# Optimization experiments

Measured on AMD Instinct MI355X. Metric: run time of the kernel, lower is better.

## Reference

```python
import jax, jax.numpy as jnp
import numpy as np

B, N, D, W = 4, 4096, 256, 7
K = 2 * W + 1  # 15 taps: positions [i-2w, ..., i]
H = 4 * D
EPS = 1e-5


def layer_norm(x, g, b):
    mu = jnp.mean(x, axis=-1, keepdims=True)
    var = jnp.mean(jnp.square(x - mu), axis=-1, keepdims=True)
    return (x - mu) * jax.lax.rsqrt(var + EPS) * g + b


def setup_inputs() -> dict:
    key = jax.random.key(0)
    ks = jax.random.split(key, 8)
    s = 0.02
    return {
        "x": jax.random.normal(ks[0], (B, N, D), dtype=jnp.float32),
        # w_mix[k] is the DxD block of the (K*D -> D) Linear acting on offset k-2w
        "w_mix": (jax.random.normal(ks[1], (K, D, D), dtype=jnp.float32) * s),
        "b_mix": jnp.zeros((D,), dtype=jnp.float32),
        "g1": jnp.ones((D,), jnp.float32) + 0.1 * jax.random.normal(ks[2], (D,), jnp.float32),
        "b1": 0.1 * jax.random.normal(ks[3], (D,), jnp.float32),
        "w_ff1": jax.random.normal(ks[4], (D, H), dtype=jnp.float32) * s,
        "b_ff1": jnp.zeros((H,), dtype=jnp.float32),
        "w_ff2": jax.random.normal(ks[5], (H, D), dtype=jnp.float32) * s,
        "b_ff2": jnp.zeros((D,), dtype=jnp.float32),
        "g2": jnp.ones((D,), jnp.float32) + 0.1 * jax.random.normal(ks[6], (D,), jnp.float32),
        "b2": 0.1 * jax.random.normal(ks[7], (D,), jnp.float32),
    }


def reference(x, w_mix, b_mix, g1, b1, w_ff1, b_ff1, w_ff2, b_ff2, g2, b2):
    # Causal windowed concat + Linear == causal 1D conv with kernel K=2w+1.
    # torch feats chunk k holds x[i - 2w + k]; conv tap k with left pad 2w
    # sees exactly x[i - 2w + k], so kernel = mix weight reshaped (K, D, D).
    mix = jax.lax.conv_general_dilated(
        x, w_mix, window_strides=(1,), padding=[(2 * W, 0)],
        dimension_numbers=("NWC", "WIO", "NWC"),
    ) + b_mix  # [B, N, D]
    # Dropout is identity in eval mode (reference baseline).
    h = layer_norm(x + mix, g1, b1)
    ff = jnp.dot(jax.nn.gelu(jnp.dot(h, w_ff1) + b_ff1, approximate=False), w_ff2) + b_ff2
    return layer_norm(h + ff, g2, b2)
```

## Files before the change

kernel.cpp:

```cpp
#include <hip/hip_runtime.h>
#include <cstdint>

#define DD     256
#define HH     1024
#define NNSEQ  4096
#define MT     32
#define XR     46
#define XPITCH 264
#define SLOTP  260
#define EPSLN  1e-5f

typedef unsigned short u16;
typedef __attribute__((ext_vector_type(8))) short short8;
typedef __attribute__((ext_vector_type(4))) float f32x4;

#define MFMA(a, b, c) __builtin_amdgcn_mfma_f32_16x16x32_bf16(a, b, c, 0, 0, 0)

__device__ __forceinline__ u16 f2bf(float f) {
  unsigned u = __float_as_uint(f);
  u += 0x7FFF + ((u >> 16) & 1);
  return (u16)(u >> 16);
}
__device__ __forceinline__ float bf2f(u16 s) { return __uint_as_float(((unsigned)s) << 16); }

__device__ __forceinline__ float fast_gelu(float v) {
  const float e = __expf(v * __builtin_fmaf(v * v, -0.0713548163f, -1.5957691216f));
  return v * __builtin_amdgcn_rcpf(1.f + e);
}

__global__ __launch_bounds__(256) void k_prep(
    const float* __restrict__ wmix, const float* __restrict__ wff1,
    const float* __restrict__ wff2, u16* __restrict__ wpk,
    u16* __restrict__ w1pk, u16* __restrict__ w2pk)
{
  const int g = blockIdx.x * 256 + threadIdx.x;
  const int u = g >> 10;
  const int t = g & 1023;
  const int fi = t >> 6, l = t & 63, q = l >> 4, cl = l & 15;
  const int n = fi * 16 + cl;
  const int r0 = q * 8;

  const float* src;
  int rowstride;
  u16* dst;
  if (u < 120) {
    src = wmix + (size_t)(u * 32 + r0) * 256 + n;
    rowstride = 256;
    dst = wpk + (size_t)u * 8192;
  } else if (u < 152) {
    const int v = u - 120, c2 = v >> 3, s = v & 7;
    src = wff1 + (size_t)(s * 32 + r0) * 1024 + c2 * 256 + n;
    rowstride = 1024;
    dst = w1pk + (size_t)v * 8192;
  } else {
    const int v = u - 152, c2 = v >> 3, s = v & 7;
    src = wff2 + (size_t)(c2 * 256 + s * 32 + r0) * 256 + n;
    rowstride = 256;
    dst = w2pk + (size_t)v * 8192;
  }

  float w[8];
#pragma unroll
  for (int j = 0; j < 8; ++j) w[j] = src[(size_t)j * rowstride];

  uint4 pk;
  unsigned* p = (unsigned*)&pk;
#pragma unroll
  for (int jj = 0; jj < 4; ++jj)
    p[jj] = (unsigned)f2bf(w[jj * 2]) | ((unsigned)f2bf(w[jj * 2 + 1]) << 16);
  *(uint4*)&dst[(size_t)fi * 512 + (size_t)l * 8] = pk;
}

__global__ __launch_bounds__(512, 4) void k_fused(
    const float* __restrict__ x, const u16* __restrict__ wpk,
    const float* __restrict__ bmix, const float* __restrict__ g1,
    const float* __restrict__ b1, const u16* __restrict__ w1pk,
    const float* __restrict__ bf1, const u16* __restrict__ w2pk,
    const float* __restrict__ bf2, const float* __restrict__ g2,
    const float* __restrict__ b2, float* __restrict__ out)
{
  __shared__ __align__(16) u16 bufA[XR * XPITCH];
  __shared__ __align__(16) u16 asbuf[2 * MT * XPITCH];
  __shared__ float redS[8][MT], redS2[8][MT];
  __shared__ float muL[MT], invL[MT];

#define bufB ((float*)asbuf)

  const int tid = threadIdx.x;
  const int wv = tid >> 6, l = tid & 63, q = l >> 4, cl = l & 15;
  const int mg = wv >> 2, ng = wv & 3;
  const long tok0 = (long)blockIdx.x * MT;
  const int n0 = (int)(tok0 & (NNSEQ - 1));

  f32x4 acc[2][4];
#pragma unroll
  for (int nt = 0; nt < 4; ++nt) {
    const float bm = (mg == 0) ? bmix[ng * 64 + nt * 16 + cl] : 0.f;
#pragma unroll
    for (int mt = 0; mt < 2; ++mt) acc[mt][nt] = (f32x4){bm, bm, bm, bm};
  }
  const u16* bbase = wpk + (size_t)(mg * 60) * 8192 + (size_t)(ng * 4) * 512 + (size_t)l * 8;

  {
    const int cslot = l * 4;
    for (int r = wv; r < XR; r += 8) {
      const int nloc = n0 - 14 + r;
      float4 v = make_float4(0.f, 0.f, 0.f, 0.f);
      if (nloc >= 0) v = *(const float4*)&x[(tok0 - 14 + r) * DD + cslot];
      uint2 pk;
      pk.x = (unsigned)f2bf(v.x) | ((unsigned)f2bf(v.y) << 16);
      pk.y = (unsigned)f2bf(v.z) | ((unsigned)f2bf(v.w) << 16);
      *(uint2*)&bufA[r * XPITCH + cslot] = pk;
    }
  }

#define LOAD_A(dst, s_)                                                         \
  {                                                                             \
    const int ks = mg * 60 + (s_);                                              \
    const int xrow = ks >> 3, c0 = (ks & 7) * 32;                               \
    _Pragma("unroll")                                                           \
    for (int mt = 0; mt < 2; ++mt)                                              \
      dst[mt] = *(const short8*)&bufA[(xrow + mt * 16 + cl) * XPITCH + c0 + q * 8]; \
  }
#define LOAD_B(dst, s_)                                                         \
  {                                                                             \
    const u16* bp = bbase + (size_t)(s_) * 8192;                                \
    _Pragma("unroll")                                                           \
    for (int nt = 0; nt < 4; ++nt)                                              \
      dst[nt] = *(const short8*)(bp + nt * 512);                                \
  }

  {
    short8 af[3][2], bfr[3][4];
    LOAD_B(bfr[0], 0)
    LOAD_B(bfr[1], 1)
    LOAD_B(bfr[2], 2)
    __syncthreads();
    LOAD_A(af[0], 0)
    LOAD_A(af[1], 1)
    LOAD_A(af[2], 2)

    for (int sb = 0; sb < 57; sb += 3) {
#pragma unroll
      for (int u = 0; u < 3; ++u) {
#pragma unroll
        for (int mt = 0; mt < 2; ++mt)
#pragma unroll
          for (int nt = 0; nt < 4; ++nt)
            acc[mt][nt] = MFMA(af[u][mt], bfr[u][nt], acc[mt][nt]);
        LOAD_A(af[u], sb + u + 3)
        LOAD_B(bfr[u], sb + u + 3)
      }
    }
#pragma unroll
    for (int u = 0; u < 3; ++u) {
#pragma unroll
      for (int mt = 0; mt < 2; ++mt)
#pragma unroll
        for (int nt = 0; nt < 4; ++nt)
          acc[mt][nt] = MFMA(af[u][mt], bfr[u][nt], acc[mt][nt]);
    }
  }
#undef LOAD_A
#undef LOAD_B

  if (mg == 1) {
#pragma unroll
    for (int mt = 0; mt < 2; ++mt)
#pragma unroll
      for (int nt = 0; nt < 4; ++nt)
#pragma unroll
        for (int reg = 0; reg < 4; ++reg)
          bufB[(mt * 16 + q * 4 + reg) * SLOTP + ng * 64 + nt * 16 + cl] = acc[mt][nt][reg];
  }
  __syncthreads();

  if (mg == 0) {
    float ps[2][4], ps2[2][4];
#pragma unroll
    for (int mt = 0; mt < 2; ++mt)
#pragma unroll
      for (int reg = 0; reg < 4; ++reg) {
        const int row = mt * 16 + q * 4 + reg;
        float s = 0.f, s2 = 0.f;
#pragma unroll
        for (int nt = 0; nt < 4; ++nt) {
          const int col = ng * 64 + nt * 16 + cl;
          const float y = acc[mt][nt][reg] + bufB[row * SLOTP + col]
                        + x[(tok0 + row) * DD + col];
          acc[mt][nt][reg] = y;
          s += y; s2 += y * y;
        }
#pragma unroll
        for (int off = 1; off < 16; off <<= 1) { s += __shfl_xor(s, off, 64); s2 += __shfl_xor(s2, off, 64); }
        ps[mt][reg] = s; ps2[mt][reg] = s2;
      }
    if (cl == 0) {
#pragma unroll
      for (int mt = 0; mt < 2; ++mt)
#pragma unroll
        for (int reg = 0; reg < 4; ++reg) {
          const int row = mt * 16 + q * 4 + reg;
          redS[ng][row] = ps[mt][reg]; redS2[ng][row] = ps2[mt][reg];
        }
    }
  }
  __syncthreads();
  if (tid < MT) {
    const float s  = redS[0][tid] + redS[1][tid] + redS[2][tid] + redS[3][tid];
    const float s2 = redS2[0][tid] + redS2[1][tid] + redS2[2][tid] + redS2[3][tid];
    const float mu = s * (1.f / DD);
    const float var = s2 * (1.f / DD) - mu * mu;
    muL[tid] = mu; invL[tid] = rsqrtf(var + EPSLN);
  }
  __syncthreads();

  if (mg == 0) {
#pragma unroll
    for (int nt = 0; nt < 4; ++nt) {
      const int col = ng * 64 + nt * 16 + cl;
      const float gv = g1[col], bv = b1[col];
#pragma unroll
      for (int mt = 0; mt < 2; ++mt)
#pragma unroll
        for (int reg = 0; reg < 4; ++reg) {
          const int row = mt * 16 + q * 4 + reg;
          const float hv = (acc[mt][nt][reg] - muL[row]) * invL[row] * gv + bv;
          bufA[row * XPITCH + col] = f2bf(hv);
        }
    }
  }
  __syncthreads();

  f32x4 acc2[2][2];
#pragma unroll
  for (int nt = 0; nt < 2; ++nt) {
    const float bv = bf2[wv * 32 + nt * 16 + cl];
#pragma unroll
    for (int mt = 0; mt < 2; ++mt) acc2[mt][nt] = (f32x4){bv, bv, bv, bv};
  }

#define FF_LDA(src, dst, s_)                                                    \
  {                                                                             \
    _Pragma("unroll")                                                           \
    for (int mt = 0; mt < 2; ++mt)                                              \
      dst[mt] = *(const short8*)&src[(mt * 16 + cl) * XPITCH + (s_) * 32 + q * 8]; \
  }
#define FF_LDB(wsrc, dst, s_)                                                   \
  {                                                                             \
    const u16* bp = wsrc + (size_t)(c * 8 + (s_)) * 8192 + (size_t)(wv * 2) * 512 + (size_t)l * 8; \
    _Pragma("unroll")                                                           \
    for (int nt = 0; nt < 2; ++nt)                                              \
      dst[nt] = *(const short8*)(bp + nt * 512);                                \
  }

  for (int c = 0; c < 4; ++c) {
    u16* asb = asbuf + (c & 1) * (MT * XPITCH);
    f32x4 acc1[2][2];
#pragma unroll
    for (int nt = 0; nt < 2; ++nt) {
      const float bv = bf1[c * 256 + wv * 32 + nt * 16 + cl];
#pragma unroll
      for (int mt = 0; mt < 2; ++mt) acc1[mt][nt] = (f32x4){bv, bv, bv, bv};
    }
    {
      short8 a2[2][2], b2r[2][2];
      FF_LDA(bufA, a2[0], 0) FF_LDB(w1pk, b2r[0], 0)
      FF_LDA(bufA, a2[1], 1) FF_LDB(w1pk, b2r[1], 1)
#pragma unroll
      for (int s = 0; s < 6; ++s) {
        const int cur = s & 1;
#pragma unroll
        for (int mt = 0; mt < 2; ++mt)
#pragma unroll
          for (int nt = 0; nt < 2; ++nt)
            acc1[mt][nt] = MFMA(a2[cur][mt], b2r[cur][nt], acc1[mt][nt]);
        FF_LDA(bufA, a2[cur], s + 2) FF_LDB(w1pk, b2r[cur], s + 2)
      }
#pragma unroll
      for (int s = 6; s < 8; ++s) {
        const int cur = s & 1;
#pragma unroll
        for (int mt = 0; mt < 2; ++mt)
#pragma unroll
          for (int nt = 0; nt < 2; ++nt)
            acc1[mt][nt] = MFMA(a2[cur][mt], b2r[cur][nt], acc1[mt][nt]);
      }
    }
#pragma unroll
    for (int mt = 0; mt < 2; ++mt)
#pragma unroll
      for (int nt = 0; nt < 2; ++nt)
#pragma unroll
        for (int reg = 0; reg < 4; ++reg) {
          const float g = fast_gelu(acc1[mt][nt][reg]);
          asb[(mt * 16 + q * 4 + reg) * XPITCH + wv * 32 + nt * 16 + cl] = f2bf(g);
        }
    __syncthreads();
    {
      short8 a2[2][2], b2r[2][2];
      FF_LDA(asb, a2[0], 0) FF_LDB(w2pk, b2r[0], 0)
      FF_LDA(asb, a2[1], 1) FF_LDB(w2pk, b2r[1], 1)
#pragma unroll
      for (int s = 0; s < 6; ++s) {
        const int cur = s & 1;
#pragma unroll
        for (int mt = 0; mt < 2; ++mt)
#pragma unroll
          for (int nt = 0; nt < 2; ++nt)
            acc2[mt][nt] = MFMA(a2[cur][mt], b2r[cur][nt], acc2[mt][nt]);
        FF_LDA(asb, a2[cur], s + 2) FF_LDB(w2pk, b2r[cur], s + 2)
      }
#pragma unroll
      for (int s = 6; s < 8; ++s) {
        const int cur = s & 1;
#pragma unroll
        for (int mt = 0; mt < 2; ++mt)
#pragma unroll
          for (int nt = 0; nt < 2; ++nt)
            acc2[mt][nt] = MFMA(a2[cur][mt], b2r[cur][nt], acc2[mt][nt]);
      }
    }
  }
#undef FF_LDA
#undef FF_LDB

  {
    float ps[2][4], ps2[2][4];
#pragma unroll
    for (int mt = 0; mt < 2; ++mt)
#pragma unroll
      for (int reg = 0; reg < 4; ++reg) {
        const int row = mt * 16 + q * 4 + reg;
        float s = 0.f, s2 = 0.f;
#pragma unroll
        for (int nt = 0; nt < 2; ++nt) {
          const int col = wv * 32 + nt * 16 + cl;
          const float y = acc2[mt][nt][reg] + bf2f(bufA[row * XPITCH + col]);
          acc2[mt][nt][reg] = y;
          s += y; s2 += y * y;
        }
#pragma unroll
        for (int off = 1; off < 16; off <<= 1) { s += __shfl_xor(s, off, 64); s2 += __shfl_xor(s2, off, 64); }
        ps[mt][reg] = s; ps2[mt][reg] = s2;
      }
    if (cl == 0) {
#pragma unroll
      for (int mt = 0; mt < 2; ++mt)
#pragma unroll
        for (int reg = 0; reg < 4; ++reg) {
          const int row = mt * 16 + q * 4 + reg;
          redS[wv][row] = ps[mt][reg]; redS2[wv][row] = ps2[mt][reg];
        }
    }
  }
  __syncthreads();
  if (tid < MT) {
    float s = 0.f, s2 = 0.f;
#pragma unroll
    for (int k = 0; k < 8; ++k) { s += redS[k][tid]; s2 += redS2[k][tid]; }
    const float mu = s * (1.f / DD);
    const float var = s2 * (1.f / DD) - mu * mu;
    muL[tid] = mu; invL[tid] = rsqrtf(var + EPSLN);
  }
  __syncthreads();

#pragma unroll
  for (int nt = 0; nt < 2; ++nt) {
    const int col = wv * 32 + nt * 16 + cl;
    const float gv = g2[col], bv = b2[col];
#pragma unroll
    for (int mt = 0; mt < 2; ++mt)
#pragma unroll
      for (int reg = 0; reg < 4; ++reg) {
        const int row = mt * 16 + q * 4 + reg;
        out[(tok0 + row) * DD + col] = (acc2[mt][nt][reg] - muL[row]) * invL[row] * gv + bv;
      }
  }
#undef bufB
}

extern "C" void kernel_launch(void* const* d_in, const int* in_sizes, int n_in,
                              void* d_out, int out_size, void* d_ws, size_t ws_size,
                              hipStream_t stream) {
  const float* x    = (const float*)d_in[0];
  const float* wmix = (const float*)d_in[1];
  const float* bmix = (const float*)d_in[2];
  const float* g1   = (const float*)d_in[3];
  const float* b1   = (const float*)d_in[4];
  const float* wff1 = (const float*)d_in[5];
  const float* bff1 = (const float*)d_in[6];
  const float* wff2 = (const float*)d_in[7];
  const float* bff2 = (const float*)d_in[8];
  const float* g2   = (const float*)d_in[9];
  const float* b2   = (const float*)d_in[10];
  float* out = (float*)d_out;

  u16* wpk  = (u16*)d_ws;
  u16* w1pk = wpk + 983040;
  u16* w2pk = w1pk + 262144;

  k_prep<<<736, 256, 0, stream>>>(wmix, wff1, wff2, wpk, w1pk, w2pk);

  k_fused<<<512, 512, 0, stream>>>(x, wpk, bmix, g1, b1,
                                   w1pk, bff1, w2pk, bff2, g2, b2, out);
}
```

Measured before the change: 153.5 us.

## Switch fused block to 32x32x16 MFMA with repacked weights and prefetch

Replaces the 16x16x32 bf16 MFMA tiling with 32x32x16 MFMA across the conv-mix, FF1 and FF2 GEMMs, and repacks the prep kernel's weight layout to match the 32-wide fragments. Each wave now issues fewer, larger MFMAs with fewer A/B fragment loads per flop. It also prefetches the next FF1/FF2 weight fragments across phase boundaries, hoists the residual x loads before the sync, and wraps the MFMAs in s_setprio. The row mapping changes, and the row reductions now need 32-lane shuffles instead of 16-lane ones.

```diff
diff --git a/kernel.cpp b/kernel.cpp
--- a/kernel.cpp
+++ b/kernel.cpp
@@ -12,9 +12,9 @@
 
 typedef unsigned short u16;
 typedef __attribute__((ext_vector_type(8))) short short8;
-typedef __attribute__((ext_vector_type(4))) float f32x4;
-
-#define MFMA(a, b, c) __builtin_amdgcn_mfma_f32_16x16x32_bf16(a, b, c, 0, 0, 0)
+typedef __attribute__((ext_vector_type(16))) float f32x16;
+
+#define MFMA32(a, b, c) __builtin_amdgcn_mfma_f32_32x32x16_bf16(a, b, c, 0, 0, 0)
 
 __device__ __forceinline__ u16 f2bf(float f) {
   unsigned u = __float_as_uint(f);
@@ -36,9 +36,10 @@
   const int g = blockIdx.x * 256 + threadIdx.x;
   const int u = g >> 10;
   const int t = g & 1023;
-  const int fi = t >> 6, l = t & 63, q = l >> 4, cl = l & 15;
-  const int n = fi * 16 + cl;
-  const int r0 = q * 8;
+  const int fp = t >> 6, l = t & 63;
+  const int gg = fp >> 1, h = fp & 1;
+  const int n = gg * 32 + (l & 31);
+  const int r0 = h * 16 + (l >> 5) * 8;
 
   const float* src;
   int rowstride;
@@ -68,7 +69,7 @@
 #pragma unroll
   for (int jj = 0; jj < 4; ++jj)
     p[jj] = (unsigned)f2bf(w[jj * 2]) | ((unsigned)f2bf(w[jj * 2 + 1]) << 16);
-  *(uint4*)&dst[(size_t)fi * 512 + (size_t)l * 8] = pk;
+  *(uint4*)&dst[(size_t)fp * 512 + (size_t)l * 8] = pk;
 }
 
 __global__ __launch_bounds__(512, 4) void k_fused(
@@ -87,19 +88,22 @@
 #define bufB ((float*)asbuf)
 
   const int tid = threadIdx.x;
-  const int wv = tid >> 6, l = tid & 63, q = l >> 4, cl = l & 15;
+  const int wv = tid >> 6, l = tid & 63;
+  const int l31 = l & 31, lh = l >> 5;
   const int mg = wv >> 2, ng = wv & 3;
   const long tok0 = (long)blockIdx.x * MT;
   const int n0 = (int)(tok0 & (NNSEQ - 1));
 
-  f32x4 acc[2][4];
-#pragma unroll
-  for (int nt = 0; nt < 4; ++nt) {
-    const float bm = (mg == 0) ? bmix[ng * 64 + nt * 16 + cl] : 0.f;
-#pragma unroll
-    for (int mt = 0; mt < 2; ++mt) acc[mt][nt] = (f32x4){bm, bm, bm, bm};
-  }
-  const u16* bbase = wpk + (size_t)(mg * 60) * 8192 + (size_t)(ng * 4) * 512 + (size_t)l * 8;
+#define ROWOF(r) (((r) & 3) + 8 * ((r) >> 2) + 4 * lh)
+
+  f32x16 acc[2];
+#pragma unroll
+  for (int nt = 0; nt < 2; ++nt) {
+    const float bm = (mg == 0) ? bmix[ng * 64 + nt * 32 + l31] : 0.f;
+#pragma unroll
+    for (int r = 0; r < 16; ++r) acc[nt][r] = bm;
+  }
+  const u16* bpkb = wpk + (size_t)(ng * 2048) + (size_t)l * 8;
 
   {
     const int cslot = l * 4;
@@ -114,95 +118,96 @@
     }
   }
 
-#define LOAD_A(dst, s_)                                                         \
+#define C_LOAD_A(dst, kg_)                                                      \
   {                                                                             \
-    const int ks = mg * 60 + (s_);                                              \
-    const int xrow = ks >> 3, c0 = (ks & 7) * 32;                               \
-    _Pragma("unroll")                                                           \
-    for (int mt = 0; mt < 2; ++mt)                                              \
-      dst[mt] = *(const short8*)&bufA[(xrow + mt * 16 + cl) * XPITCH + c0 + q * 8]; \
-  }
-#define LOAD_B(dst, s_)                                                         \
+    const int tap = (kg_) >> 4, c0 = ((kg_) & 15) * 16;                         \
+    dst = *(const short8*)&bufA[(tap + l31) * XPITCH + c0 + lh * 8];            \
+  }
+#define C_LOAD_B(dst, kg_)                                                      \
   {                                                                             \
-    const u16* bp = bbase + (size_t)(s_) * 8192;                                \
-    _Pragma("unroll")                                                           \
-    for (int nt = 0; nt < 4; ++nt)                                              \
-      dst[nt] = *(const short8*)(bp + nt * 512);                                \
-  }
-
-  {
-    short8 af[3][2], bfr[3][4];
-    LOAD_B(bfr[0], 0)
-    LOAD_B(bfr[1], 1)
-    LOAD_B(bfr[2], 2)
+    const u16* bp = bpkb + (size_t)((kg_) >> 1) * 8192 + (size_t)((kg_) & 1) * 512; \
+    dst[0] = *(const short8*)bp;                                                \
+    dst[1] = *(const short8*)(bp + 1024);                                       \
+  }
+
+  {
+    const int kg0 = mg * 120;
+    short8 af[4], bfr[4][2];
+    C_LOAD_B(bfr[0], kg0 + 0)
+    C_LOAD_B(bfr[1], kg0 + 1)
+    C_LOAD_B(bfr[2], kg0 + 2)
+    C_LOAD_B(bfr[3], kg0 + 3)
     __syncthreads();
-    LOAD_A(af[0], 0)
-    LOAD_A(af[1], 1)
-    LOAD_A(af[2], 2)
-
-    for (int sb = 0; sb < 57; sb += 3) {
-#pragma unroll
-      for (int u = 0; u < 3; ++u) {
-#pragma unroll
-        for (int mt = 0; mt < 2; ++mt)
-#pragma unroll
-          for (int nt = 0; nt < 4; ++nt)
-            acc[mt][nt] = MFMA(af[u][mt], bfr[u][nt], acc[mt][nt]);
-        LOAD_A(af[u], sb + u + 3)
-        LOAD_B(bfr[u], sb + u + 3)
-      }
-    }
-#pragma unroll
-    for (int u = 0; u < 3; ++u) {
-#pragma unroll
-      for (int mt = 0; mt < 2; ++mt)
-#pragma unroll
-        for (int nt = 0; nt < 4; ++nt)
-          acc[mt][nt] = MFMA(af[u][mt], bfr[u][nt], acc[mt][nt]);
-    }
-  }
-#undef LOAD_A
-#undef LOAD_B
+    C_LOAD_A(af[0], kg0 + 0)
+    C_LOAD_A(af[1], kg0 + 1)
+    C_LOAD_A(af[2], kg0 + 2)
+    C_LOAD_A(af[3], kg0 + 3)
+
+    for (int sb = 0; sb < 116; sb += 4) {
+#pragma unroll
+      for (int u = 0; u < 4; ++u) {
+        __builtin_amdgcn_s_setprio(1);
+        acc[0] = MFMA32(af[u], bfr[u][0], acc[0]);
+        acc[1] = MFMA32(af[u], bfr[u][1], acc[1]);
+        __builtin_amdgcn_s_setprio(0);
+        C_LOAD_A(af[u], kg0 + sb + u + 4)
+        C_LOAD_B(bfr[u], kg0 + sb + u + 4)
+      }
+    }
+#pragma unroll
+    for (int u = 0; u < 4; ++u) {
+      __builtin_amdgcn_s_setprio(1);
+      acc[0] = MFMA32(af[u], bfr[u][0], acc[0]);
+      acc[1] = MFMA32(af[u], bfr[u][1], acc[1]);
+      __builtin_amdgcn_s_setprio(0);
+    }
+  }
+#undef C_LOAD_A
+#undef C_LOAD_B
+
+  float xres[2][16];
+  if (mg == 0) {
+#pragma unroll
+    for (int r = 0; r < 16; ++r) {
+      const int row = ROWOF(r);
+      const float* xp = &x[(tok0 + row) * DD + ng * 64 + l31];
+      xres[0][r] = xp[0];
+      xres[1][r] = xp[32];
+    }
+  }
 
   if (mg == 1) {
 #pragma unroll
-    for (int mt = 0; mt < 2; ++mt)
-#pragma unroll
-      for (int nt = 0; nt < 4; ++nt)
-#pragma unroll
-        for (int reg = 0; reg < 4; ++reg)
-          bufB[(mt * 16 + q * 4 + reg) * SLOTP + ng * 64 + nt * 16 + cl] = acc[mt][nt][reg];
+    for (int nt = 0; nt < 2; ++nt)
+#pragma unroll
+      for (int r = 0; r < 16; ++r)
+        bufB[ROWOF(r) * SLOTP + ng * 64 + nt * 32 + l31] = acc[nt][r];
   }
   __syncthreads();
 
   if (mg == 0) {
-    float ps[2][4], ps2[2][4];
-#pragma unroll
-    for (int mt = 0; mt < 2; ++mt)
-#pragma unroll
-      for (int reg = 0; reg < 4; ++reg) {
-        const int row = mt * 16 + q * 4 + reg;
-        float s = 0.f, s2 = 0.f;
-#pragma unroll
-        for (int nt = 0; nt < 4; ++nt) {
-          const int col = ng * 64 + nt * 16 + cl;
-          const float y = acc[mt][nt][reg] + bufB[row * SLOTP + col]
-                        + x[(tok0 + row) * DD + col];
-          acc[mt][nt][reg] = y;
-          s += y; s2 += y * y;
-        }
-#pragma unroll
-        for (int off = 1; off < 16; off <<= 1) { s += __shfl_xor(s, off, 64); s2 += __shfl_xor(s2, off, 64); }
-        ps[mt][reg] = s; ps2[mt][reg] = s2;
-      }
-    if (cl == 0) {
-#pragma unroll
-      for (int mt = 0; mt < 2; ++mt)
-#pragma unroll
-        for (int reg = 0; reg < 4; ++reg) {
-          const int row = mt * 16 + q * 4 + reg;
-          redS[ng][row] = ps[mt][reg]; redS2[ng][row] = ps2[mt][reg];
-        }
+    float ps[16], ps2[16];
+#pragma unroll
+    for (int r = 0; r < 16; ++r) {
+      const int row = ROWOF(r);
+      float s = 0.f, s2 = 0.f;
+#pragma unroll
+      for (int nt = 0; nt < 2; ++nt) {
+        const int col = ng * 64 + nt * 32 + l31;
+        const float y = acc[nt][r] + bufB[row * SLOTP + col] + xres[nt][r];
+        acc[nt][r] = y;
+        s += y; s2 += y * y;
+      }
+#pragma unroll
+      for (int off = 1; off < 32; off <<= 1) { s += __shfl_xor(s, off, 64); s2 += __shfl_xor(s2, off, 64); }
+      ps[r] = s; ps2[r] = s2;
+    }
+    if (l31 == 0) {
+#pragma unroll
+      for (int r = 0; r < 16; ++r) {
+        const int row = ROWOF(r);
+        redS[ng][row] = ps[r]; redS2[ng][row] = ps2[r];
+      }
     }
   }
   __syncthreads();
@@ -215,143 +220,124 @@
   }
   __syncthreads();
 
+#define F_LDA(src, dst, s_)                                                     \
+    dst = *(const short8*)&src[l31 * XPITCH + (s_) * 16 + lh * 8];
+#define F_LDB(wsrc, dst, c_, s_)                                                \
+    dst = *(const short8*)(wsrc + (size_t)((c_) * 8 + ((s_) >> 1)) * 8192       \
+                          + (size_t)(wv * 2 + ((s_) & 1)) * 512 + (size_t)l * 8);
+
+  short8 pb1[3];
+  F_LDB(w1pk, pb1[0], 0, 0)
+  F_LDB(w1pk, pb1[1], 0, 1)
+  F_LDB(w1pk, pb1[2], 0, 2)
+
   if (mg == 0) {
 #pragma unroll
-    for (int nt = 0; nt < 4; ++nt) {
-      const int col = ng * 64 + nt * 16 + cl;
+    for (int nt = 0; nt < 2; ++nt) {
+      const int col = ng * 64 + nt * 32 + l31;
       const float gv = g1[col], bv = b1[col];
 #pragma unroll
-      for (int mt = 0; mt < 2; ++mt)
-#pragma unroll
-        for (int reg = 0; reg < 4; ++reg) {
-          const int row = mt * 16 + q * 4 + reg;
-          const float hv = (acc[mt][nt][reg] - muL[row]) * invL[row] * gv + bv;
-          bufA[row * XPITCH + col] = f2bf(hv);
-        }
-    }
-  }
-  __syncthreads();
-
-  f32x4 acc2[2][2];
-#pragma unroll
-  for (int nt = 0; nt < 2; ++nt) {
-    const float bv = bf2[wv * 32 + nt * 16 + cl];
-#pragma unroll
-    for (int mt = 0; mt < 2; ++mt) acc2[mt][nt] = (f32x4){bv, bv, bv, bv};
-  }
-
-#define FF_LDA(src, dst, s_)                                                    \
-  {                                                                             \
-    _Pragma("unroll")                                                           \
-    for (int mt = 0; mt < 2; ++mt)                                              \
-      dst[mt] = *(const short8*)&src[(mt * 16 + cl) * XPITCH + (s_) * 32 + q * 8]; \
-  }
-#define FF_LDB(wsrc, dst, s_)                                                   \
-  {                                                                             \
-    const u16* bp = wsrc + (size_t)(c * 8 + (s_)) * 8192 + (size_t)(wv * 2) * 512 + (size_t)l * 8; \
-    _Pragma("unroll")                                                           \
-    for (int nt = 0; nt < 2; ++nt)                                              \
-      dst[nt] = *(const short8*)(bp + nt * 512);                                \
+      for (int r = 0; r < 16; ++r) {
+        const int row = ROWOF(r);
+        bufA[row * XPITCH + col] = f2bf((acc[nt][r] - muL[row]) * invL[row] * gv + bv);
+      }
+    }
+  }
+  __syncthreads();
+
+  f32x16 acc2;
+  {
+    const float bv = bf2[wv * 32 + l31];
+#pragma unroll
+    for (int r = 0; r < 16; ++r) acc2[r] = bv;
   }
 
   for (int c = 0; c < 4; ++c) {
     u16* asb = asbuf + (c & 1) * (MT * XPITCH);
-    f32x4 acc1[2][2];
-#pragma unroll
-    for (int nt = 0; nt < 2; ++nt) {
-      const float bv = bf1[c * 256 + wv * 32 + nt * 16 + cl];
-#pragma unroll
-      for (int mt = 0; mt < 2; ++mt) acc1[mt][nt] = (f32x4){bv, bv, bv, bv};
-    }
+    f32x16 acc1;
     {
-      short8 a2[2][2], b2r[2][2];
-      FF_LDA(bufA, a2[0], 0) FF_LDB(w1pk, b2r[0], 0)
-      FF_LDA(bufA, a2[1], 1) FF_LDB(w1pk, b2r[1], 1)
-#pragma unroll
-      for (int s = 0; s < 6; ++s) {
-        const int cur = s & 1;
-#pragma unroll
-        for (int mt = 0; mt < 2; ++mt)
-#pragma unroll
-          for (int nt = 0; nt < 2; ++nt)
-            acc1[mt][nt] = MFMA(a2[cur][mt], b2r[cur][nt], acc1[mt][nt]);
-        FF_LDA(bufA, a2[cur], s + 2) FF_LDB(w1pk, b2r[cur], s + 2)
-      }
-#pragma unroll
-      for (int s = 6; s < 8; ++s) {
-        const int cur = s & 1;
-#pragma unroll
-        for (int mt = 0; mt < 2; ++mt)
-#pragma unroll
-          for (int nt = 0; nt < 2; ++nt)
-            acc1[mt][nt] = MFMA(a2[cur][mt], b2r[cur][nt], acc1[mt][nt]);
-      }
-    }
-#pragma unroll
-    for (int mt = 0; mt < 2; ++mt)
-#pragma unroll
-      for (int nt = 0; nt < 2; ++nt)
-#pragma unroll
-        for (int reg = 0; reg < 4; ++reg) {
-          const float g = fast_gelu(acc1[mt][nt][reg]);
-          asb[(mt * 16 + q * 4 + reg) * XPITCH + wv * 32 + nt * 16 + cl] = f2bf(g);
-        }
+      const float bv = bf1[c * 256 + wv * 32 + l31];
+#pragma unroll
+      for (int r = 0; r < 16; ++r) acc1[r] = bv;
+    }
+    {
+      short8 a3[3], b3[3];
+      F_LDA(bufA, a3[0], 0) b3[0] = pb1[0];
+      F_LDA(bufA, a3[1], 1) b3[1] = pb1[1];
+      F_LDA(bufA, a3[2], 2) b3[2] = pb1[2];
+#pragma unroll
+      for (int s = 0; s < 13; ++s) {
+        const int cur = s % 3;
+        __builtin_amdgcn_s_setprio(1);
+        acc1 = MFMA32(a3[cur], b3[cur], acc1);
+        __builtin_amdgcn_s_setprio(0);
+        F_LDA(bufA, a3[cur], s + 3)
+        F_LDB(w1pk, b3[cur], c, s + 3)
+      }
+      __builtin_amdgcn_s_setprio(1);
+#pragma unroll
+      for (int s = 13; s < 16; ++s)
+        acc1 = MFMA32(a3[s % 3], b3[s % 3], acc1);
+      __builtin_amdgcn_s_setprio(0);
+    }
+    short8 pb2[3];
+    F_LDB(w2pk, pb2[0], c, 0)
+    F_LDB(w2pk, pb2[1], c, 1)
+    F_LDB(w2pk, pb2[2], c, 2)
+#pragma unroll
+    for (int r = 0; r < 16; ++r) {
+      const float g = fast_gelu(acc1[r]);
+      asb[ROWOF(r) * XPITCH + wv * 32 + l31] = f2bf(g);
+    }
+    if (c < 3) {
+      F_LDB(w1pk, pb1[0], c + 1, 0)
+      F_LDB(w1pk, pb1[1], c + 1, 1)
+      F_LDB(w1pk, pb1[2], c + 1, 2)
+    }
     __syncthreads();
     {
-      short8 a2[2][2], b2r[2][2];
-      FF_LDA(asb, a2[0], 0) FF_LDB(w2pk, b2r[0], 0)
-      FF_LDA(asb, a2[1], 1) FF_LDB(w2pk, b2r[1], 1)
-#pragma unroll
-      for (int s = 0; s < 6; ++s) {
-        const int cur = s & 1;
-#pragma unroll
-        for (int mt = 0; mt < 2; ++mt)
-#pragma unroll
-          for (int nt = 0; nt < 2; ++nt)
-            acc2[mt][nt] = MFMA(a2[cur][mt], b2r[cur][nt], acc2[mt][nt]);
-        FF_LDA(asb, a2[cur], s + 2) FF_LDB(w2pk, b2r[cur], s + 2)
-      }
-#pragma unroll
-      for (int s = 6; s < 8; ++s) {
-        const int cur = s & 1;
-#pragma unroll
-        for (int mt = 0; mt < 2; ++mt)
-#pragma unroll
-          for (int nt = 0; nt < 2; ++nt)
-            acc2[mt][nt] = MFMA(a2[cur][mt], b2r[cur][nt], acc2[mt][nt]);
-      }
-    }
-  }
-#undef FF_LDA
-#undef FF_LDB
-
-  {
-    float ps[2][4], ps2[2][4];
-#pragma unroll
-    for (int mt = 0; mt < 2; ++mt)
-#pragma unroll
-      for (int reg = 0; reg < 4; ++reg) {
-        const int row = mt * 16 + q * 4 + reg;
-        float s = 0.f, s2 = 0.f;
-#pragma unroll
-        for (int nt = 0; nt < 2; ++nt) {
-          const int col = wv * 32 + nt * 16 + cl;
-          const float y = acc2[mt][nt][reg] + bf2f(bufA[row * XPITCH + col]);
-          acc2[mt][nt][reg] = y;
-          s += y; s2 += y * y;
-        }
-#pragma unroll
-        for (int off = 1; off < 16; off <<= 1) { s += __shfl_xor(s, off, 64); s2 += __shfl_xor(s2, off, 64); }
-        ps[mt][reg] = s; ps2[mt][reg] = s2;
-      }
-    if (cl == 0) {
-#pragma unroll
-      for (int mt = 0; mt < 2; ++mt)
-#pragma unroll
-        for (int reg = 0; reg < 4; ++reg) {
-          const int row = mt * 16 + q * 4 + reg;
-          redS[wv][row] = ps[mt][reg]; redS2[wv][row] = ps2[mt][reg];
-        }
+      short8 a3[3], b3[3];
+      F_LDA(asb, a3[0], 0) b3[0] = pb2[0];
+      F_LDA(asb, a3[1], 1) b3[1] = pb2[1];
+      F_LDA(asb, a3[2], 2) b3[2] = pb2[2];
+#pragma unroll
+      for (int s = 0; s < 13; ++s) {
+        const int cur = s % 3;
+        __builtin_amdgcn_s_setprio(1);
+        acc2 = MFMA32(a3[cur], b3[cur], acc2);
+        __builtin_amdgcn_s_setprio(0);
+        F_LDA(asb, a3[cur], s + 3)
+        F_LDB(w2pk, b3[cur], c, s + 3)
+      }
+      __builtin_amdgcn_s_setprio(1);
+#pragma unroll
+      for (int s = 13; s < 16; ++s)
+        acc2 = MFMA32(a3[s % 3], b3[s % 3], acc2);
+      __builtin_amdgcn_s_setprio(0);
+    }
+  }
+#undef F_LDA
+#undef F_LDB
+
+  {
+    float ps[16], ps2[16];
+    const int col = wv * 32 + l31;
+#pragma unroll
+    for (int r = 0; r < 16; ++r) {
+      const int row = ROWOF(r);
+      const float y = acc2[r] + bf2f(bufA[row * XPITCH + col]);
+      acc2[r] = y;
+      float s = y, s2 = y * y;
+#pragma unroll
+      for (int off = 1; off < 32; off <<= 1) { s += __shfl_xor(s, off, 64); s2 += __shfl_xor(s2, off, 64); }
+      ps[r] = s; ps2[r] = s2;
+    }
+    if (l31 == 0) {
+#pragma unroll
+      for (int r = 0; r < 16; ++r) {
+        const int row = ROWOF(r);
+        redS[wv][row] = ps[r]; redS2[wv][row] = ps2[r];
+      }
     }
   }
   __syncthreads();
@@ -365,18 +351,16 @@
   }
   __syncthreads();
 
-#pragma unroll
-  for (int nt = 0; nt < 2; ++nt) {
-    const int col = wv * 32 + nt * 16 + cl;
+  {
+    const int col = wv * 32 + l31;
     const float gv = g2[col], bv = b2[col];
 #pragma unroll
-    for (int mt = 0; mt < 2; ++mt)
-#pragma unroll
-      for (int reg = 0; reg < 4; ++reg) {
-        const int row = mt * 16 + q * 4 + reg;
-        out[(tok0 + row) * DD + col] = (acc2[mt][nt][reg] - muL[row]) * invL[row] * gv + bv;
-      }
-  }
+    for (int r = 0; r < 16; ++r) {
+      const int row = ROWOF(r);
+      out[(tok0 + row) * DD + col] = (acc2[r] - muL[row]) * invL[row] * gv + bv;
+    }
+  }
+#undef ROWOF
 #undef bufB
 }
 
```

Result: slower. 162.2 us (+5.6%).
